# Kernel optimization log

Measured on AMD Instinct MI355X. Metric: run time of the kernel, lower is better.

Reference implementation:

```python
import jax, jax.numpy as jnp
import numpy as np

B, C, H, W = 4, 128, 64, 64


def setup_inputs() -> dict:
    key = jax.random.key(0)
    ks = jax.random.split(key, 7)
    s = 1.0 / np.sqrt(C)
    return {
        "x": jax.random.normal(ks[0], (B, C, H, W), dtype=jnp.float32),
        "Wq": jax.random.normal(ks[1], (C, C), dtype=jnp.float32) * s,
        "bq": jnp.zeros((C,), dtype=jnp.float32),
        "Wk": jax.random.normal(ks[2], (C, C), dtype=jnp.float32) * s,
        "bk": jnp.zeros((C,), dtype=jnp.float32),
        "Wv": jax.random.normal(ks[3], (C, C), dtype=jnp.float32) * s,
        "bv": jnp.zeros((C,), dtype=jnp.float32),
    }


def reference(x, Wq, bq, Wk, bk, Wv, bv):
    b, c, h, w = x.shape
    n = h * w
    scale = c ** (-0.5)
    # tokens: [B, N, C]
    xt = x.reshape(b, c, n).transpose(0, 2, 1)
    # 1x1 convs == per-token channel GEMMs (out[c'] = sum_c W[c',c] x[c] + b[c'])
    q = jnp.einsum("bnc,dc->bnd", xt, Wq) + bq  # [B, N, C]
    k = jnp.einsum("bnc,dc->bnd", xt, Wk) + bk  # [B, N, C]
    v = jnp.einsum("bnc,dc->bnd", xt, Wv) + bv  # [B, N, C]
    scores = jnp.einsum("bic,bjc->bij", q, k) * scale  # [B, N, N]
    attn = jax.nn.softmax(scores, axis=-1)
    out = jnp.einsum("bij,bjc->bic", attn, v)  # [B, N, C]
    return out.transpose(0, 2, 1).reshape(b, c, h, w)
```

## Files before the change

kernel.cpp:

```cpp
#include <hip/hip_runtime.h>
#include <hip/hip_bf16.h>


#define BATCH 4
#define CH    128
#define NTOK  4096
#define TK    64
#define SCALE 0.08838834764831845f
#define LOG2E 1.4426950408889634f
#define MFIX  16.0f

typedef __attribute__((ext_vector_type(8)))  short short8;
typedef __attribute__((ext_vector_type(4)))  float f32x4;
typedef __attribute__((ext_vector_type(16))) float f32x16;

static __device__ __forceinline__ unsigned short f2bf(float f) {
    __hip_bfloat16 h = (__hip_bfloat16)f;
    return *(const unsigned short*)&h;
}

static __device__ __forceinline__ unsigned cvt_pk_bf16(float lo, float hi) {
    unsigned r;
    asm("v_cvt_pk_bf16_f32 %0, %1, %2" : "=v"(r) : "v"(lo), "v"(hi));
    return r;
}

__global__ __launch_bounds__(256) void convert_w_kernel(
    const float* __restrict__ Wq, const float* __restrict__ Wk,
    const float* __restrict__ Wv, unsigned short* __restrict__ wb)
{
    const int idx = (blockIdx.x * 256 + threadIdx.x) * 4;
    const float* srcs[3] = {Wq, Wk, Wv};
    #pragma unroll
    for (int m = 0; m < 3; ++m) {
        float4 v = *(const float4*)(srcs[m] + idx);
        unsigned short o[4] = {f2bf(v.x), f2bf(v.y), f2bf(v.z), f2bf(v.w)};
        *(uint2*)(wb + (size_t)m * CH * CH + idx) = *(const uint2*)o;
    }
}

__global__ __launch_bounds__(256) void proj_mfma_kernel(
    const float* __restrict__ x,
    const unsigned short* __restrict__ wb_all,
    const float* __restrict__ bq, const float* __restrict__ bk,
    const float* __restrict__ bv,
    unsigned short* __restrict__ q_ws, unsigned short* __restrict__ k_ws,
    unsigned short* __restrict__ vt_ws)
{
    __shared__ __align__(16) unsigned short XsT[64 * CH];
    __shared__ __align__(16) unsigned short Ep[128 * 72];

    const int t    = threadIdx.x;
    const int w    = t >> 6;
    const int lane = t & 63;
    const int quad = lane >> 4;
    const int c16  = lane & 15;
    const int n0   = blockIdx.x * 64;
    const int b    = blockIdx.y;
    const int z    = blockIdx.z;
    const float* xb = x + (size_t)b * CH * NTOK;

    {
        const int tok = lane;
        #pragma unroll
        for (int cc = 0; cc < 4; ++cc) {
            const int cb = 32 * w + 8 * cc;
            unsigned short tmp[8];
            #pragma unroll
            for (int j = 0; j < 8; ++j)
                tmp[j] = f2bf(xb[(size_t)(cb + j) * NTOK + n0 + tok]);
            const int phys = ((cb >> 3) ^ (tok & 15));
            *(short8*)&XsT[tok * CH + phys * 8] = *(const short8*)tmp;
        }
    }
    __syncthreads();

    if (z < 2) {
        const unsigned short* wm = wb_all + (size_t)z * CH * CH;
        const float* bias = (z == 0) ? bq : bk;
        unsigned short* dst = (z == 0) ? q_ws : k_ws;
        const float mul = (z == 0) ? (SCALE * LOG2E) : 1.0f;

        short8 xa[4];
        #pragma unroll
        for (int ks = 0; ks < 4; ++ks)
            xa[ks] = *(const short8*)&XsT[(16 * w + c16) * CH + (((4 * ks + quad) ^ c16) << 3)];

        #pragma unroll
        for (int nt = 0; nt < 8; ++nt) {
            f32x4 a = (f32x4){0.f, 0.f, 0.f, 0.f};
            const unsigned short* wr = wm + (16 * nt + c16) * CH;
            #pragma unroll
            for (int ks = 0; ks < 4; ++ks) {
                const short8 bf = *(const short8*)(wr + 32 * ks + 8 * quad);
                a = __builtin_amdgcn_mfma_f32_16x16x32_bf16(xa[ks], bf, a, 0, 0, 0);
            }
            const float bvv = bias[16 * nt + c16];
            #pragma unroll
            for (int r = 0; r < 4; ++r) {
                const int tok = 16 * w + quad * 4 + r;
                Ep[tok * 136 + 16 * nt + c16] = f2bf((a[r] + bvv) * mul);
            }
        }
        __syncthreads();
        #pragma unroll
        for (int p = 0; p < 4; ++p) {
            const int tok = p * 16 + (t >> 4);
            const int u   = t & 15;
            const uint4 v = *(const uint4*)&Ep[tok * 136 + u * 8];
            *(uint4*)&dst[((size_t)b * NTOK + n0 + tok) * CH + u * 8] = v;
        }
    } else {
        const unsigned short* wvb = wb_all + (size_t)2 * CH * CH;
        short8 wva[2][4];
        float  bvv[2][4];
        #pragma unroll
        for (int mt = 0; mt < 2; ++mt) {
            const int crow16 = 16 * (2 * w + mt);
            #pragma unroll
            for (int ks = 0; ks < 4; ++ks)
                wva[mt][ks] = *(const short8*)&wvb[(crow16 + c16) * CH + 32 * ks + 8 * quad];
            #pragma unroll
            for (int r = 0; r < 4; ++r)
                bvv[mt][r] = bv[crow16 + quad * 4 + r];
        }
        #pragma unroll
        for (int nt = 0; nt < 4; ++nt) {
            short8 xbf[4];
            #pragma unroll
            for (int ks = 0; ks < 4; ++ks)
                xbf[ks] = *(const short8*)&XsT[(16 * nt + c16) * CH + (((4 * ks + quad) ^ c16) << 3)];
            #pragma unroll
            for (int mt = 0; mt < 2; ++mt) {
                f32x4 acc = (f32x4){0.f, 0.f, 0.f, 0.f};
                #pragma unroll
                for (int ks = 0; ks < 4; ++ks)
                    acc = __builtin_amdgcn_mfma_f32_16x16x32_bf16(wva[mt][ks], xbf[ks], acc, 0, 0, 0);
                #pragma unroll
                for (int r = 0; r < 4; ++r) {
                    const int crow = 16 * (2 * w + mt) + quad * 4 + r;
                    Ep[crow * 72 + 16 * nt + c16] = f2bf(acc[r] + bvv[mt][r]);
                }
            }
        }
        __syncthreads();
        #pragma unroll
        for (int p = 0; p < 4; ++p) {
            const int c = p * 32 + (t >> 3);
            const int u = t & 7;
            const uint4 v = *(const uint4*)&Ep[c * 72 + u * 8];
            *(uint4*)&vt_ws[((size_t)b * CH + c) * NTOK + n0 + u * 8] = v;
        }
    }
}

template <int SPLIT>
__global__ __launch_bounds__(256, 2) void flash_attn_mfma(
    const unsigned short* __restrict__ q_ws,
    const unsigned short* __restrict__ k_ws,
    const unsigned short* __restrict__ vt_ws,
    float* __restrict__ out,
    float* __restrict__ Op, float* __restrict__ l_p)
{
    __shared__ __align__(16) unsigned short KsU[2][TK * CH];
    __shared__ __align__(16) unsigned short VtU[2][CH * TK];

    const int t    = threadIdx.x;
    const int w    = t >> 6;
    const int lane = t & 63;
    const int half = lane >> 5;
    const int l32  = lane & 31;
    const int jc   = blockIdx.y;
    const int b    = blockIdx.z;
    const int n0   = blockIdx.x * 128;
    const int jbeg = jc * (NTOK / SPLIT);
    constexpr int NT = (NTOK / SPLIT) / TK;

    const unsigned short* kg = k_ws  + (size_t)b * NTOK * CH;
    const unsigned short* vg = vt_ws + (size_t)b * CH * NTOK;

    short8 qa[8];
    {
        const unsigned short* qrow =
            q_ws + ((size_t)b * NTOK + n0 + 32 * w + l32) * CH;
        #pragma unroll
        for (int ks = 0; ks < 8; ++ks)
            qa[ks] = *(const short8*)(qrow + ks * 16 + half * 8);
    }

    f32x16 Oa[4];
    #pragma unroll
    for (int ct = 0; ct < 4; ++ct) Oa[ct] = (f32x16)(0.0f);
    float lsum = 0.f;

    const int krl = lane >> 4, ku = lane & 15;
    const int vcl = lane >> 3, vu = lane & 7;

    auto STAGE = [&](int buf, int jj) {
        #pragma unroll
        for (int ci = 0; ci < 4; ++ci) {
            const int row = 16 * w + 4 * ci + krl;
            const int g   = ku ^ (row & 15);
            const unsigned short* src = kg + (size_t)(jj + row) * CH + g * 8;
            __builtin_amdgcn_global_load_lds(
                (const __attribute__((address_space(1))) void*)src,
                (__attribute__((address_space(3))) void*)&KsU[buf][(16 * w + 4 * ci) * CH],
                16, 0, 0);
        }
        #pragma unroll
        for (int ci = 0; ci < 4; ++ci) {
            const int c = 32 * w + 8 * ci + vcl;
            const int g = vu ^ (c & 7);
            const unsigned short* src = vg + (size_t)c * NTOK + jj + g * 8;
            __builtin_amdgcn_global_load_lds(
                (const __attribute__((address_space(1))) void*)src,
                (__attribute__((address_space(3))) void*)&VtU[buf][(32 * w + 8 * ci) * TK],
                16, 0, 0);
        }
    };

    STAGE(0, jbeg);

    int j0 = jbeg;
    for (int tt = 0; tt < NT; ++tt, j0 += TK) {
        const int cur = tt & 1;
        if (tt + 1 < NT) {
            STAGE(cur ^ 1, j0 + TK);
            asm volatile("s_waitcnt vmcnt(8)" ::: "memory");
        } else {
            asm volatile("s_waitcnt vmcnt(0)" ::: "memory");
        }
        __builtin_amdgcn_sched_barrier(0);
        __builtin_amdgcn_s_barrier();
        __builtin_amdgcn_sched_barrier(0);

        const unsigned short* Kc = &KsU[cur][0];
        const unsigned short* Vc = &VtU[cur][0];

        f32x16 s[2];
        s[0] = (f32x16)(-MFIX);
        s[1] = (f32x16)(-MFIX);
        __builtin_amdgcn_s_setprio(1);
        #pragma unroll
        for (int ks = 0; ks < 8; ++ks) {
            const int ph = (2 * ks + half) ^ (l32 & 15);
            const short8 kf0 = *(const short8*)&Kc[l32 * CH + ph * 8];
            const short8 kf1 = *(const short8*)&Kc[(32 + l32) * CH + ph * 8];
            s[0] = __builtin_amdgcn_mfma_f32_32x32x16_bf16(kf0, qa[ks], s[0], 0, 0, 0);
            s[1] = __builtin_amdgcn_mfma_f32_32x32x16_bf16(kf1, qa[ks], s[1], 0, 0, 0);
        }
        __builtin_amdgcn_s_setprio(0);

        short8 pb[4];
        #pragma unroll
        for (int kt = 0; kt < 2; ++kt) {
            float p[16];
            #pragma unroll
            for (int r = 0; r < 16; ++r) p[r] = exp2f(s[kt][r]);
            float a0 = 0.f, a1 = 0.f, a2 = 0.f, a3 = 0.f;
            #pragma unroll
            for (int r = 0; r < 4; ++r) {
                a0 += p[r]; a1 += p[4 + r]; a2 += p[8 + r]; a3 += p[12 + r];
            }
            lsum += (a0 + a1) + (a2 + a3);
            unsigned wd[8];
            #pragma unroll
            for (int i = 0; i < 8; ++i) wd[i] = cvt_pk_bf16(p[2 * i], p[2 * i + 1]);
            auto r02 = __builtin_amdgcn_permlane32_swap(wd[0], wd[2], false, false);
            auto r13 = __builtin_amdgcn_permlane32_swap(wd[1], wd[3], false, false);
            auto r46 = __builtin_amdgcn_permlane32_swap(wd[4], wd[6], false, false);
            auto r57 = __builtin_amdgcn_permlane32_swap(wd[5], wd[7], false, false);
            union { unsigned u[4]; short8 s8; } f0, f1;
            f0.u[0] = r02[0]; f0.u[1] = r13[0]; f0.u[2] = r02[1]; f0.u[3] = r13[1];
            f1.u[0] = r46[0]; f1.u[1] = r57[0]; f1.u[2] = r46[1]; f1.u[3] = r57[1];
            pb[2 * kt + 0] = f0.s8;
            pb[2 * kt + 1] = f1.s8;
        }

        __builtin_amdgcn_s_setprio(1);
        #pragma unroll
        for (int ks2 = 0; ks2 < 4; ++ks2) {
            #pragma unroll
            for (int ct = 0; ct < 4; ++ct) {
                const int ch = 32 * ct + l32;
                const int ph = (2 * ks2 + half) ^ (ch & 7);
                const short8 vf = *(const short8*)&VtU[cur][ch * TK + ph * 8];
                Oa[ct] = __builtin_amdgcn_mfma_f32_32x32x16_bf16(vf, pb[ks2], Oa[ct], 0, 0, 0);
            }
        }
        __builtin_amdgcn_s_setprio(0);
        (void)Vc;
        __builtin_amdgcn_sched_barrier(0);
        __builtin_amdgcn_s_barrier();
        __builtin_amdgcn_sched_barrier(0);
    }

    const float lt = lsum + __shfl_xor(lsum, 32);
    const int n = n0 + 32 * w + l32;

    if constexpr (SPLIT == 1) {
        const float inv = 1.0f / lt;
        #pragma unroll
        for (int ct = 0; ct < 4; ++ct) {
            #pragma unroll
            for (int r = 0; r < 16; ++r) {
                const int c = 32 * ct + (r & 3) + 8 * (r >> 2) + 4 * half;
                out[((size_t)b * CH + c) * NTOK + n] = Oa[ct][r] * inv;
            }
        }
    } else {
        const size_t chunk = (size_t)(b * SPLIT + jc);
        #pragma unroll
        for (int ct = 0; ct < 4; ++ct) {
            #pragma unroll
            for (int r = 0; r < 16; ++r) {
                const int c = 32 * ct + (r & 3) + 8 * (r >> 2) + 4 * half;
                Op[(chunk * CH + c) * NTOK + n] = Oa[ct][r];
            }
        }
        if (half == 0) l_p[chunk * NTOK + n] = lt;
    }
}

template <int SPLIT>
__global__ __launch_bounds__(256) void combine_kernel(
    const float* __restrict__ Op, const float* __restrict__ l_p,
    float* __restrict__ out)
{
    const int b = blockIdx.y;
    const size_t idx = ((size_t)blockIdx.x * 256 + threadIdx.x) * 4;
    const int c = (int)(idx >> 12);
    const int n = (int)(idx & (NTOK - 1));
    float4 acc = make_float4(0.f, 0.f, 0.f, 0.f);
    float4 den = make_float4(0.f, 0.f, 0.f, 0.f);
    #pragma unroll
    for (int j = 0; j < SPLIT; ++j) {
        const size_t chunk = (size_t)(b * SPLIT + j);
        const float4 o = *(const float4*)&Op[(chunk * CH + c) * NTOK + n];
        const float4 d = *(const float4*)&l_p[chunk * NTOK + n];
        acc.x += o.x; acc.y += o.y; acc.z += o.z; acc.w += o.w;
        den.x += d.x; den.y += d.y; den.z += d.z; den.w += d.w;
    }
    float4 r;
    r.x = acc.x / den.x; r.y = acc.y / den.y;
    r.z = acc.z / den.z; r.w = acc.w / den.w;
    *(float4*)&out[((size_t)b * CH * NTOK) + idx] = r;
}

extern "C" void kernel_launch(void* const* d_in, const int* in_sizes, int n_in,
                              void* d_out, int out_size, void* d_ws, size_t ws_size,
                              hipStream_t stream) {
    const float* x  = (const float*)d_in[0];
    const float* Wq = (const float*)d_in[1];
    const float* bq = (const float*)d_in[2];
    const float* Wk = (const float*)d_in[3];
    const float* bk = (const float*)d_in[4];
    const float* Wv = (const float*)d_in[5];
    const float* bv = (const float*)d_in[6];
    float* out = (float*)d_out;

    const size_t QKV = (size_t)BATCH * NTOK * CH;
    unsigned short* q_ws  = (unsigned short*)d_ws;
    unsigned short* k_ws  = q_ws + QKV;
    unsigned short* vt_ws = k_ws + QKV;
    unsigned short* wb    = vt_ws + QKV;
    float* Op = (float*)(wb + 3 * CH * CH);

    const size_t baseBytes = 3 * QKV * 2 + 3 * CH * CH * 2;
    auto needBytes = [&](size_t S) {
        return baseBytes + S * BATCH * NTOK * (size_t)(CH * 4 + 4);
    };

    convert_w_kernel<<<CH * CH / (256 * 4), 256, 0, stream>>>(Wq, Wk, Wv, wb);

    dim3 gp(NTOK / 64, BATCH, 3);
    proj_mfma_kernel<<<gp, 256, 0, stream>>>(x, wb, bq, bk, bv, q_ws, k_ws, vt_ws);

    dim3 gc(CH * NTOK / 1024, BATCH);
    if (ws_size >= needBytes(4)) {
        float* l_p = Op + (size_t)4 * BATCH * NTOK * CH;
        dim3 ga(NTOK / 128, 4, BATCH);
        flash_attn_mfma<4><<<ga, 256, 0, stream>>>(q_ws, k_ws, vt_ws, out, Op, l_p);
        combine_kernel<4><<<gc, 256, 0, stream>>>(Op, l_p, out);
    } else if (ws_size >= needBytes(2)) {
        float* l_p = Op + (size_t)2 * BATCH * NTOK * CH;
        dim3 ga(NTOK / 128, 2, BATCH);
        flash_attn_mfma<2><<<ga, 256, 0, stream>>>(q_ws, k_ws, vt_ws, out, Op, l_p);
        combine_kernel<2><<<gc, 256, 0, stream>>>(Op, l_p, out);
    } else {
        dim3 ga(NTOK / 128, 1, BATCH);
        flash_attn_mfma<1><<<ga, 256, 0, stream>>>(q_ws, k_ws, vt_ws, out,
                                                   nullptr, nullptr);
    }
}
```

Baseline: 133.7 us.

## Fuse weight conversion into projection, split KV six ways, single-buffer K

Drops the separate weight-conversion kernel; the projection kernel now reads fp32 weights directly and packs them to bf16 in registers, saving one launch and a workspace round trip. The attention kernel can now split the key/value range six ways, with uneven tile counts per chunk, to give more blocks for occupancy. K staging goes to a single LDS buffer: the loads for the next tile are issued only after the QK^T step has finished and a barrier has passed, which frees LDS but makes K loads overlap less with compute. The setprio hints are removed, and the larger split adds more partial-output traffic for the combine kernel.

Result: slower. 142.7 us (+6.7%).

```diff
diff --git a/kernel.cpp b/kernel.cpp
--- a/kernel.cpp
+++ b/kernel.cpp
@@ -6,6 +6,7 @@
 #define CH    128
 #define NTOK  4096
 #define TK    64
+#define TILES (NTOK / TK)
 #define SCALE 0.08838834764831845f
 #define LOG2E 1.4426950408889634f
 #define MFIX  16.0f
@@ -25,23 +26,19 @@
     return r;
 }
 
-__global__ __launch_bounds__(256) void convert_w_kernel(
-    const float* __restrict__ Wq, const float* __restrict__ Wk,
-    const float* __restrict__ Wv, unsigned short* __restrict__ wb)
-{
-    const int idx = (blockIdx.x * 256 + threadIdx.x) * 4;
-    const float* srcs[3] = {Wq, Wk, Wv};
-    #pragma unroll
-    for (int m = 0; m < 3; ++m) {
-        float4 v = *(const float4*)(srcs[m] + idx);
-        unsigned short o[4] = {f2bf(v.x), f2bf(v.y), f2bf(v.z), f2bf(v.w)};
-        *(uint2*)(wb + (size_t)m * CH * CH + idx) = *(const uint2*)o;
-    }
+static __device__ __forceinline__ short8 pack_bf16x8(float4 a, float4 b) {
+    union { unsigned u[4]; short8 s8; } f;
+    f.u[0] = cvt_pk_bf16(a.x, a.y);
+    f.u[1] = cvt_pk_bf16(a.z, a.w);
+    f.u[2] = cvt_pk_bf16(b.x, b.y);
+    f.u[3] = cvt_pk_bf16(b.z, b.w);
+    return f.s8;
 }
 
 __global__ __launch_bounds__(256) void proj_mfma_kernel(
     const float* __restrict__ x,
-    const unsigned short* __restrict__ wb_all,
+    const float* __restrict__ Wq, const float* __restrict__ Wk,
+    const float* __restrict__ Wv,
     const float* __restrict__ bq, const float* __restrict__ bk,
     const float* __restrict__ bv,
     unsigned short* __restrict__ q_ws, unsigned short* __restrict__ k_ws,
@@ -76,7 +73,7 @@
     __syncthreads();
 
     if (z < 2) {
-        const unsigned short* wm = wb_all + (size_t)z * CH * CH;
+        const float* wm = (z == 0) ? Wq : Wk;
         const float* bias = (z == 0) ? bq : bk;
         unsigned short* dst = (z == 0) ? q_ws : k_ws;
         const float mul = (z == 0) ? (SCALE * LOG2E) : 1.0f;
@@ -89,10 +86,13 @@
         #pragma unroll
         for (int nt = 0; nt < 8; ++nt) {
             f32x4 a = (f32x4){0.f, 0.f, 0.f, 0.f};
-            const unsigned short* wr = wm + (16 * nt + c16) * CH;
+            const float* wr = wm + (16 * nt + c16) * CH;
             #pragma unroll
             for (int ks = 0; ks < 4; ++ks) {
-                const short8 bf = *(const short8*)(wr + 32 * ks + 8 * quad);
+                const float* wp = wr + 32 * ks + 8 * quad;
+                const float4 w0 = *(const float4*)wp;
+                const float4 w1 = *(const float4*)(wp + 4);
+                const short8 bf = pack_bf16x8(w0, w1);
                 a = __builtin_amdgcn_mfma_f32_16x16x32_bf16(xa[ks], bf, a, 0, 0, 0);
             }
             const float bvv = bias[16 * nt + c16];
@@ -111,15 +111,18 @@
             *(uint4*)&dst[((size_t)b * NTOK + n0 + tok) * CH + u * 8] = v;
         }
     } else {
-        const unsigned short* wvb = wb_all + (size_t)2 * CH * CH;
         short8 wva[2][4];
         float  bvv[2][4];
         #pragma unroll
         for (int mt = 0; mt < 2; ++mt) {
             const int crow16 = 16 * (2 * w + mt);
             #pragma unroll
-            for (int ks = 0; ks < 4; ++ks)
-                wva[mt][ks] = *(const short8*)&wvb[(crow16 + c16) * CH + 32 * ks + 8 * quad];
+            for (int ks = 0; ks < 4; ++ks) {
+                const float* wp = Wv + (crow16 + c16) * CH + 32 * ks + 8 * quad;
+                const float4 w0 = *(const float4*)wp;
+                const float4 w1 = *(const float4*)(wp + 4);
+                wva[mt][ks] = pack_bf16x8(w0, w1);
+            }
             #pragma unroll
             for (int r = 0; r < 4; ++r)
                 bvv[mt][r] = bv[crow16 + quad * 4 + r];
@@ -162,7 +165,7 @@
     float* __restrict__ out,
     float* __restrict__ Op, float* __restrict__ l_p)
 {
-    __shared__ __align__(16) unsigned short KsU[2][TK * CH];
+    __shared__ __align__(16) unsigned short KsU[TK * CH];
     __shared__ __align__(16) unsigned short VtU[2][CH * TK];
 
     const int t    = threadIdx.x;
@@ -173,8 +176,11 @@
     const int jc   = blockIdx.y;
     const int b    = blockIdx.z;
     const int n0   = blockIdx.x * 128;
-    const int jbeg = jc * (NTOK / SPLIT);
-    constexpr int NT = (NTOK / SPLIT) / TK;
+
+    constexpr int cbase = TILES / SPLIT;
+    constexpr int crem  = TILES % SPLIT;
+    const int myt = cbase + (jc < crem ? 1 : 0);
+    const int t0  = jc * cbase + (jc < crem ? jc : crem);
 
     const unsigned short* kg = k_ws  + (size_t)b * NTOK * CH;
     const unsigned short* vg = vt_ws + (size_t)b * CH * NTOK;
@@ -196,7 +202,7 @@
     const int krl = lane >> 4, ku = lane & 15;
     const int vcl = lane >> 3, vu = lane & 7;
 
-    auto STAGE = [&](int buf, int jj) {
+    auto K_DMA = [&](int jj) {
         #pragma unroll
         for (int ci = 0; ci < 4; ++ci) {
             const int row = 16 * w + 4 * ci + krl;
@@ -204,9 +210,11 @@
             const unsigned short* src = kg + (size_t)(jj + row) * CH + g * 8;
             __builtin_amdgcn_global_load_lds(
                 (const __attribute__((address_space(1))) void*)src,
-                (__attribute__((address_space(3))) void*)&KsU[buf][(16 * w + 4 * ci) * CH],
+                (__attribute__((address_space(3))) void*)&KsU[(16 * w + 4 * ci) * CH],
                 16, 0, 0);
         }
+    };
+    auto V_DMA = [&](int buf, int jj) {
         #pragma unroll
         for (int ci = 0; ci < 4; ++ci) {
             const int c = 32 * w + 8 * ci + vcl;
@@ -219,37 +227,34 @@
         }
     };
 
-    STAGE(0, jbeg);
-
-    int j0 = jbeg;
-    for (int tt = 0; tt < NT; ++tt, j0 += TK) {
+    K_DMA(t0 * TK);
+    V_DMA(0, t0 * TK);
+
+    for (int tt = 0; tt < myt; ++tt) {
         const int cur = tt & 1;
-        if (tt + 1 < NT) {
-            STAGE(cur ^ 1, j0 + TK);
-            asm volatile("s_waitcnt vmcnt(8)" ::: "memory");
-        } else {
-            asm volatile("s_waitcnt vmcnt(0)" ::: "memory");
-        }
+        asm volatile("s_waitcnt vmcnt(0)" ::: "memory");
         __builtin_amdgcn_sched_barrier(0);
         __builtin_amdgcn_s_barrier();
         __builtin_amdgcn_sched_barrier(0);
 
-        const unsigned short* Kc = &KsU[cur][0];
-        const unsigned short* Vc = &VtU[cur][0];
-
         f32x16 s[2];
         s[0] = (f32x16)(-MFIX);
         s[1] = (f32x16)(-MFIX);
-        __builtin_amdgcn_s_setprio(1);
         #pragma unroll
         for (int ks = 0; ks < 8; ++ks) {
             const int ph = (2 * ks + half) ^ (l32 & 15);
-            const short8 kf0 = *(const short8*)&Kc[l32 * CH + ph * 8];
-            const short8 kf1 = *(const short8*)&Kc[(32 + l32) * CH + ph * 8];
+            const short8 kf0 = *(const short8*)&KsU[l32 * CH + ph * 8];
+            const short8 kf1 = *(const short8*)&KsU[(32 + l32) * CH + ph * 8];
             s[0] = __builtin_amdgcn_mfma_f32_32x32x16_bf16(kf0, qa[ks], s[0], 0, 0, 0);
             s[1] = __builtin_amdgcn_mfma_f32_32x32x16_bf16(kf1, qa[ks], s[1], 0, 0, 0);
         }
-        __builtin_amdgcn_s_setprio(0);
+        __builtin_amdgcn_sched_barrier(0);
+        __builtin_amdgcn_s_barrier();
+        __builtin_amdgcn_sched_barrier(0);
+        if (tt + 1 < myt) {
+            K_DMA((t0 + tt + 1) * TK);
+            V_DMA(cur ^ 1, (t0 + tt + 1) * TK);
+        }
 
         short8 pb[4];
         #pragma unroll
@@ -277,22 +282,17 @@
             pb[2 * kt + 1] = f1.s8;
         }
 
-        __builtin_amdgcn_s_setprio(1);
+        const unsigned short* Vc = &VtU[cur][0];
         #pragma unroll
         for (int ks2 = 0; ks2 < 4; ++ks2) {
             #pragma unroll
             for (int ct = 0; ct < 4; ++ct) {
                 const int ch = 32 * ct + l32;
                 const int ph = (2 * ks2 + half) ^ (ch & 7);
-                const short8 vf = *(const short8*)&VtU[cur][ch * TK + ph * 8];
+                const short8 vf = *(const short8*)&Vc[ch * TK + ph * 8];
                 Oa[ct] = __builtin_amdgcn_mfma_f32_32x32x16_bf16(vf, pb[ks2], Oa[ct], 0, 0, 0);
             }
         }
-        __builtin_amdgcn_s_setprio(0);
-        (void)Vc;
-        __builtin_amdgcn_sched_barrier(0);
-        __builtin_amdgcn_s_barrier();
-        __builtin_amdgcn_sched_barrier(0);
     }
 
     const float lt = lsum + __shfl_xor(lsum, 32);
@@ -363,30 +363,28 @@
     unsigned short* q_ws  = (unsigned short*)d_ws;
     unsigned short* k_ws  = q_ws + QKV;
     unsigned short* vt_ws = k_ws + QKV;
-    unsigned short* wb    = vt_ws + QKV;
-    float* Op = (float*)(wb + 3 * CH * CH);
-
-    const size_t baseBytes = 3 * QKV * 2 + 3 * CH * CH * 2;
+    float* Op = (float*)(vt_ws + QKV);
+
+    const size_t baseBytes = 3 * QKV * 2;
     auto needBytes = [&](size_t S) {
         return baseBytes + S * BATCH * NTOK * (size_t)(CH * 4 + 4);
     };
 
-    convert_w_kernel<<<CH * CH / (256 * 4), 256, 0, stream>>>(Wq, Wk, Wv, wb);
-
     dim3 gp(NTOK / 64, BATCH, 3);
-    proj_mfma_kernel<<<gp, 256, 0, stream>>>(x, wb, bq, bk, bv, q_ws, k_ws, vt_ws);
+    proj_mfma_kernel<<<gp, 256, 0, stream>>>(x, Wq, Wk, Wv, bq, bk, bv,
+                                             q_ws, k_ws, vt_ws);
 
     dim3 gc(CH * NTOK / 1024, BATCH);
-    if (ws_size >= needBytes(4)) {
+    if (ws_size >= needBytes(6)) {
+        float* l_p = Op + (size_t)6 * BATCH * NTOK * CH;
+        dim3 ga(NTOK / 128, 6, BATCH);
+        flash_attn_mfma<6><<<ga, 256, 0, stream>>>(q_ws, k_ws, vt_ws, out, Op, l_p);
+        combine_kernel<6><<<gc, 256, 0, stream>>>(Op, l_p, out);
+    } else if (ws_size >= needBytes(4)) {
         float* l_p = Op + (size_t)4 * BATCH * NTOK * CH;
         dim3 ga(NTOK / 128, 4, BATCH);
         flash_attn_mfma<4><<<ga, 256, 0, stream>>>(q_ws, k_ws, vt_ws, out, Op, l_p);
         combine_kernel<4><<<gc, 256, 0, stream>>>(Op, l_p, out);
-    } else if (ws_size >= needBytes(2)) {
-        float* l_p = Op + (size_t)2 * BATCH * NTOK * CH;
-        dim3 ga(NTOK / 128, 2, BATCH);
-        flash_attn_mfma<2><<<ga, 256, 0, stream>>>(q_ws, k_ws, vt_ws, out, Op, l_p);
-        combine_kernel<2><<<gc, 256, 0, stream>>>(Op, l_p, out);
     } else {
         dim3 ga(NTOK / 128, 1, BATCH);
         flash_attn_mfma<1><<<ga, 256, 0, stream>>>(q_ws, k_ws, vt_ws, out,
```
